# Performance work log

Hardware: AMD Instinct MI355X
Metric: run time of the kernel (lower is better)

Reference implementation:

```python
import jax, jax.numpy as jnp
import numpy as np

N_NODES = 500_000
N_EDGES = 1_000_000
EMB = 64           # config.Model.embedding_size
F = 128            # config.Model.latency_feature_size
L = 8              # config.Latency.latency_feature_length
OP_CNT = 5000
SV_CNT = 2000
ST_CNT = 16
IN_DIM = 3 * EMB + L  # 200


def setup_inputs() -> dict:
    key = jax.random.key(0)
    ks = jax.random.split(key, 24)
    s = 0.02
    inp = {
        'operation_id': jax.random.randint(ks[0], (N_NODES,), 0, OP_CNT, dtype=jnp.int32),
        'service_id':   jax.random.randint(ks[1], (N_NODES,), 0, SV_CNT, dtype=jnp.int32),
        'status_id':    jax.random.randint(ks[2], (N_NODES,), 0, ST_CNT, dtype=jnp.int32),
        'latency_feat': jax.random.normal(ks[3], (N_NODES, L), dtype=jnp.float32),
        'edge_src':     jax.random.randint(ks[4], (N_EDGES,), 0, N_NODES, dtype=jnp.int32),
        'edge_dst':     jax.random.randint(ks[5], (N_EDGES,), 0, N_NODES, dtype=jnp.int32),
        'eps':          jax.random.normal(ks[6], (N_NODES, F), dtype=jnp.float32),
        # parameters (LevelEmbedding + TreeLSTMLatencyEncoder + TreeLSTMLatencyDecoder)
        'op_embed':      jax.random.normal(ks[7],  (OP_CNT, EMB), dtype=jnp.float32) * s,
        'service_embed': jax.random.normal(ks[8],  (SV_CNT, EMB), dtype=jnp.float32) * s,
        'status_embed':  jax.random.normal(ks[9],  (ST_CNT, EMB), dtype=jnp.float32) * s,
        'enc_W1': jax.random.normal(ks[10], (IN_DIM, F), dtype=jnp.float32) * s,
        'enc_b1': jnp.zeros((F,), dtype=jnp.float32),
        'enc_W2': jax.random.normal(ks[11], (F, 2 * F), dtype=jnp.float32) * s,
        'enc_b2': jnp.zeros((2 * F,), dtype=jnp.float32),
        'dec_Wself': jax.random.normal(ks[12], (F, F), dtype=jnp.float32) * s,
        'dec_Wagg':  jax.random.normal(ks[13], (F, F), dtype=jnp.float32) * s,
        'mu_W': jax.random.normal(ks[14], (F, L), dtype=jnp.float32) * s,
        'mu_b': jnp.zeros((L,), dtype=jnp.float32),
        'lv_W': jax.random.normal(ks[15], (F, L), dtype=jnp.float32) * s,
        'lv_b': jnp.zeros((L,), dtype=jnp.float32),
        'opwise_embed': jax.random.normal(ks[16], (OP_CNT + 1, 2 * L * L), dtype=jnp.float32) * s,
    }
    return inp


def reference(operation_id, service_id, status_id, latency_feat, edge_src, edge_dst, eps,
              op_embed, service_embed, status_embed,
              enc_W1, enc_b1, enc_W2, enc_b2,
              dec_Wself, dec_Wagg, mu_W, mu_b, lv_W, lv_b, opwise_embed):
    N = latency_feat.shape[0]
    # ---- LevelEmbedding: gathers + concat ----
    feats = jnp.concatenate([
        op_embed[operation_id],
        service_embed[service_id],
        status_embed[status_id],
        latency_feat,
    ], axis=-1)  # [N, 3*EMB + L]
    # ---- TreeLSTMLatencyEncoder ----
    h = jax.nn.relu(feats @ enc_W1 + enc_b1)
    y = h @ enc_W2 + enc_b2                       # [N, 2F]
    z_mu, z_lv = jnp.split(y, 2, axis=-1)
    z_lv = jnp.tanh(z_lv)
    z = z_mu + jnp.exp(0.5 * z_lv) * eps          # reparameterize, [N, F]
    # ---- TreeLSTM decoder (one child-sum message-passing step over edges) ----
    agg = jax.ops.segment_sum(z[edge_src], edge_dst, num_segments=N)  # scatter-reduce
    yd = jax.nn.relu(z @ dec_Wself + agg @ dec_Wagg)                  # [N, F]
    mu = yd @ mu_W + mu_b   # [N, L]
    lv = yd @ lv_W + lv_b   # [N, L]
    # op-wise output transform: per-node [1,L] @ [L,L]
    w = opwise_embed[operation_id].reshape(N, L, 2 * L)
    w_mu, w_lv = w[..., :L], w[..., L:]
    mu = jnp.einsum('nl,nlk->nk', mu, w_mu)
    lv = jnp.einsum('nl,nlk->nk', lv, w_lv)
    # ---- latency_loss: gaussian NLL + opid scatter aggregation ----
    label = latency_feat
    loss = (mu - label) ** 2 / (2.0 * jnp.exp(lv) + 1e-7) + 0.5 * lv  # [N, L]
    loss_node = jnp.mean(loss, axis=1)                                 # [N]
    op_loss = jax.ops.segment_sum(loss_node, operation_id, num_segments=OP_CNT)
    op_cnt = jax.ops.segment_sum(jnp.ones((N,), jnp.int32), operation_id, num_segments=OP_CNT)
    lat_loss = jnp.mean(loss_node)
    kl = -0.5 * jnp.mean(z_lv + 1.0 - jnp.exp(z_lv) - z_mu ** 2)
    total = lat_loss + kl
    return (total, op_loss, op_cnt)
```

## Files before the change

### kernel.cpp

```cpp
#include <hip/hip_runtime.h>
#include <math.h>

#define NN 500000
#define NE 1000000
#define OPC 5000
#define NBLK_SCAN 489
#define NBLK ((NN + 127) / 128)

typedef short short8 __attribute__((ext_vector_type(8)));
typedef float f32x4 __attribute__((ext_vector_type(4)));

static __device__ __forceinline__ short f2bf(float f) {
    unsigned u = __builtin_bit_cast(unsigned, f);
    u += 0x7fffu + ((u >> 16) & 1u);
    return (short)(u >> 16);
}
static __device__ __forceinline__ float bf2f(short s) {
    unsigned u = ((unsigned)(unsigned short)s) << 16;
    return __builtin_bit_cast(float, u);
}
static __device__ __forceinline__ short8 cvt8(float4 a, float4 b) {
    short8 r;
    r[0] = f2bf(a.x); r[1] = f2bf(a.y); r[2] = f2bf(a.z); r[3] = f2bf(a.w);
    r[4] = f2bf(b.x); r[5] = f2bf(b.y); r[6] = f2bf(b.z); r[7] = f2bf(b.w);
    return r;
}
static __device__ __forceinline__ short8 ldcvt(const float* p) {
    const float4* p4 = (const float4*)p;
    return cvt8(p4[0], p4[1]);
}

__global__ void prep_kernel(const float* __restrict__ W1, const float* __restrict__ W2,
                            const float* __restrict__ Wself, const float* __restrict__ Wagg,
                            const float* __restrict__ muW, const float* __restrict__ lvW,
                            short* __restrict__ W1s, short* __restrict__ W2s,
                            short* __restrict__ Wds0, short* __restrict__ Wds1,
                            short* __restrict__ HWp)
{
    int idx = blockIdx.x * 256 + threadIdx.x;
    {
        int col = idx >> 8, r = idx & 255;
        int k = ((r >> 3) ^ (col & 7)) * 8 + (r & 7);
        W1s[idx] = (k < 200) ? f2bf(W1[k * 128 + col]) : (short)0;
    }
    {
        int col = idx >> 7, r = idx & 127;
        int k = ((r >> 3) ^ (col & 7)) * 8 + (r & 7);
        W2s[idx] = f2bf(W2[k * 256 + col]);
    }
    if (idx < 128 * 128) {
        int col = idx >> 7, r = idx & 127;
        int k = ((r >> 3) ^ (col & 7)) * 8 + (r & 7);
        Wds0[idx] = f2bf(Wself[k * 128 + col]);
        Wds1[idx] = f2bf(Wagg[k * 128 + col]);
    }
    if (idx < 16 * 128) {
        int n = idx >> 7, k = idx & 127;
        HWp[idx] = (n < 8) ? f2bf(muW[k * 8 + n]) : f2bf(lvW[k * 8 + (n - 8)]);
    }
}

__global__ __launch_bounds__(256, 2) void enc1_mfma(
    const int* __restrict__ op_id, const int* __restrict__ sv_id, const int* __restrict__ st_id,
    const float* __restrict__ lat,
    const float* __restrict__ opE, const float* __restrict__ svE, const float* __restrict__ stE,
    const short* __restrict__ W1s, const float* __restrict__ b1,
    short* __restrict__ h_bf)
{
    __shared__ __align__(16) short Bb[128 * 256];
    const int tid = threadIdx.x;
    const int lane = tid & 63, w = tid >> 6;
    const int m = lane & 15, q = lane >> 4;
    const int bbase = blockIdx.x * 128;
    const int wbase = bbase + w * 32;
    const bool wv = (wbase < NN);

    {
        const short8* g = (const short8*)W1s;
        short8* l = (short8*)Bb;
        #pragma unroll
        for (int i = 0; i < 16; i++) l[tid + 256 * i] = g[tid + 256 * i];
    }
    __syncthreads();

    f32x4 acc[2][8];
    #pragma unroll
    for (int a2 = 0; a2 < 2; a2++)
        #pragma unroll
        for (int nf = 0; nf < 8; nf++) acc[a2][nf] = (f32x4)0.0f;

    if (wv) {
        const int n0 = wbase + m, n1 = wbase + 16 + m;
        const size_t op0 = (size_t)op_id[n0] * 64, op1 = (size_t)op_id[n1] * 64;
        const size_t sv0 = (size_t)sv_id[n0] * 64, sv1 = (size_t)sv_id[n1] * 64;
        const size_t st0 = (size_t)st_id[n0] * 64, st1 = (size_t)st_id[n1] * 64;

        #pragma unroll
        for (int s = 0; s < 7; s++) {
            short8 a0, a1;
            if (s < 2) {
                a0 = ldcvt(opE + op0 + s * 32 + q * 8);
                a1 = ldcvt(opE + op1 + s * 32 + q * 8);
            } else if (s < 4) {
                a0 = ldcvt(svE + sv0 + (s - 2) * 32 + q * 8);
                a1 = ldcvt(svE + sv1 + (s - 2) * 32 + q * 8);
            } else if (s < 6) {
                a0 = ldcvt(stE + st0 + (s - 4) * 32 + q * 8);
                a1 = ldcvt(stE + st1 + (s - 4) * 32 + q * 8);
            } else {
                if (q == 0) {
                    a0 = ldcvt(lat + (size_t)n0 * 8);
                    a1 = ldcvt(lat + (size_t)n1 * 8);
                } else {
                    #pragma unroll
                    for (int i = 0; i < 8; i++) { a0[i] = 0; a1[i] = 0; }
                }
            }
            const int slot = ((4 * s + q) ^ (m & 7)) * 8;
            #pragma unroll
            for (int nf = 0; nf < 8; nf++) {
                const short8 b = *(const short8*)&Bb[(nf * 16 + m) * 256 + slot];
                acc[0][nf] = __builtin_amdgcn_mfma_f32_16x16x32_bf16(a0, b, acc[0][nf], 0, 0, 0);
                acc[1][nf] = __builtin_amdgcn_mfma_f32_16x16x32_bf16(a1, b, acc[1][nf], 0, 0, 0);
            }
        }
    }
    __syncthreads();

    if (wv) {
        #pragma unroll
        for (int nf = 0; nf < 8; nf++) {
            int col = nf * 16 + m;
            float bb = b1[col];
            #pragma unroll
            for (int a2 = 0; a2 < 2; a2++)
                #pragma unroll
                for (int r = 0; r < 4; r++) {
                    int g = w * 32 + a2 * 16 + q * 4 + r;
                    Bb[g * 136 + col] = f2bf(fmaxf(acc[a2][nf][r] + bb, 0.0f));
                }
        }
    }
    __syncthreads();

    {
        int g = tid >> 1, cb = (tid & 1) * 64;
        int node = bbase + g;
        if (node < NN) {
            short8* dst = (short8*)(h_bf + (size_t)node * 128 + cb);
            const short8* src = (const short8*)&Bb[g * 136 + cb];
            #pragma unroll
            for (int i = 0; i < 8; i++) dst[i] = src[i];
        }
    }
}

__global__ __launch_bounds__(256, 2) void enc2_mfma(
    const short* __restrict__ h_bf, const short* __restrict__ W2s, const float* __restrict__ b2,
    const float* __restrict__ eps, short* __restrict__ z_bf, float* __restrict__ kl_sum)
{
    __shared__ __align__(16) short Bb[256 * 128];
    int* ldsI = (int*)Bb;
    const int tid = threadIdx.x;
    const int lane = tid & 63, w = tid >> 6;
    const int m = lane & 15, q = lane >> 4;
    const int bbase = blockIdx.x * 128;
    const int wbase = bbase + w * 32;
    const bool wv = (wbase < NN);

    {
        const short8* g8 = (const short8*)W2s;
        short8* l = (short8*)Bb;
        #pragma unroll
        for (int i = 0; i < 16; i++) l[tid + 256 * i] = g8[tid + 256 * i];
    }
    __syncthreads();

    f32x4 acc[2][16];
    #pragma unroll
    for (int a2 = 0; a2 < 2; a2++)
        #pragma unroll
        for (int nf = 0; nf < 16; nf++) acc[a2][nf] = (f32x4)0.0f;

    if (wv) {
        short8 a[2][4];
        #pragma unroll
        for (int s = 0; s < 4; s++) {
            a[0][s] = *(const short8*)(h_bf + (size_t)(wbase + m) * 128 + s * 32 + q * 8);
            a[1][s] = *(const short8*)(h_bf + (size_t)(wbase + 16 + m) * 128 + s * 32 + q * 8);
        }
        #pragma unroll
        for (int s = 0; s < 4; s++) {
            const int slot = ((4 * s + q) ^ (m & 7)) * 8;
            #pragma unroll
            for (int nf = 0; nf < 16; nf++) {
                const short8 b = *(const short8*)&Bb[(nf * 16 + m) * 128 + slot];
                acc[0][nf] = __builtin_amdgcn_mfma_f32_16x16x32_bf16(a[0][s], b, acc[0][nf], 0, 0, 0);
                acc[1][nf] = __builtin_amdgcn_mfma_f32_16x16x32_bf16(a[1][s], b, acc[1][nf], 0, 0, 0);
            }
        }
    }
    __syncthreads();

    float kll = 0.0f;
    #pragma unroll
    for (int a2 = 0; a2 < 2; a2++) {
        if (wv) {
            #pragma unroll
            for (int nf = 0; nf < 8; nf++) {
                int col = nf * 16 + m;
                float bm = b2[col], bl = b2[col + 128];
                #pragma unroll
                for (int r = 0; r < 4; r++) {
                    float mu = acc[a2][nf][r] + bm;
                    float lr = acc[a2][nf + 8][r] + bl;
                    float e2 = __expf(2.0f * lr);
                    float t  = 1.0f - 2.0f * __builtin_amdgcn_rcpf(e2 + 1.0f);
                    float s  = __expf(0.5f * t);
                    kll += t + 1.0f - s * s - mu * mu;
                    int pk = (int)(unsigned short)f2bf(mu)
                           | ((int)(unsigned short)f2bf(s) << 16);
                    ldsI[(w * 16 + q * 4 + r) * 132 + col] = pk;
                }
            }
        }
        __syncthreads();
        {
            int g = tid >> 2, cb = (tid & 3) * 32;
            int node = bbase + (g >> 4) * 32 + a2 * 16 + (g & 15);
            if (node < NN) {
                const float4* ep = (const float4*)(eps + (size_t)node * 128 + cb);
                const int4*   lp = (const int4*)&ldsI[g * 132 + cb];
                #pragma unroll
                for (int c = 0; c < 4; c++) {
                    int4 va = lp[c * 2], vb = lp[c * 2 + 1];
                    float4 ea = ep[c * 2], eb = ep[c * 2 + 1];
                    short8 o;
                    o[0] = f2bf(fmaf(bf2f((short)(va.x >> 16)), ea.x, bf2f((short)va.x)));
                    o[1] = f2bf(fmaf(bf2f((short)(va.y >> 16)), ea.y, bf2f((short)va.y)));
                    o[2] = f2bf(fmaf(bf2f((short)(va.z >> 16)), ea.z, bf2f((short)va.z)));
                    o[3] = f2bf(fmaf(bf2f((short)(va.w >> 16)), ea.w, bf2f((short)va.w)));
                    o[4] = f2bf(fmaf(bf2f((short)(vb.x >> 16)), eb.x, bf2f((short)vb.x)));
                    o[5] = f2bf(fmaf(bf2f((short)(vb.y >> 16)), eb.y, bf2f((short)vb.y)));
                    o[6] = f2bf(fmaf(bf2f((short)(vb.z >> 16)), eb.z, bf2f((short)vb.z)));
                    o[7] = f2bf(fmaf(bf2f((short)(vb.w >> 16)), eb.w, bf2f((short)vb.w)));
                    *(short8*)(z_bf + (size_t)node * 128 + cb + c * 8) = o;
                }
            }
        }
        __syncthreads();
    }
    #pragma unroll
    for (int off = 32; off > 0; off >>= 1) kll += __shfl_down(kll, off);
    if (lane == 0) atomicAdd(kl_sum, kll);
}

__global__ void hist_kernel(const int* __restrict__ edst, int* __restrict__ cnt)
{
    int e = blockIdx.x * 256 + threadIdx.x;
    if (e < NE) atomicAdd(&cnt[edst[e]], 1);
}

__global__ void scan1_kernel(const int* __restrict__ cnt, int* __restrict__ bsum)
{
    __shared__ int ls[256];
    int b = blockIdx.x, tid = threadIdx.x;
    int idx0 = b * 1024 + tid * 4;
    int s = 0;
    #pragma unroll
    for (int i = 0; i < 4; i++) { int idx = idx0 + i; if (idx < NN) s += cnt[idx]; }
    ls[tid] = s; __syncthreads();
    for (int off = 128; off > 0; off >>= 1) {
        if (tid < off) ls[tid] += ls[tid + off];
        __syncthreads();
    }
    if (tid == 0) bsum[b] = ls[0];
}

__global__ void scan2_kernel(int* __restrict__ bsum, int* __restrict__ rowstart)
{
    __shared__ int ls[512];
    int tid = threadIdx.x;
    int v = (tid < NBLK_SCAN) ? bsum[tid] : 0;
    ls[tid] = v; __syncthreads();
    for (int off = 1; off < 512; off <<= 1) {
        int t = 0;
        if (tid >= off) t = ls[tid - off];
        __syncthreads();
        ls[tid] += t;
        __syncthreads();
    }
    if (tid < NBLK_SCAN) bsum[tid] = (tid == 0) ? 0 : ls[tid - 1];
    if (tid == 0) rowstart[NN] = NE;
}

__global__ void scan3_kernel(const int* __restrict__ cnt, const int* __restrict__ bsum,
                             int* __restrict__ rowstart, int* __restrict__ cursor)
{
    __shared__ int ls[256];
    int b = blockIdx.x, tid = threadIdx.x;
    int idx0 = b * 1024 + tid * 4;
    int v[4]; int s = 0;
    #pragma unroll
    for (int i = 0; i < 4; i++) { int idx = idx0 + i; v[i] = (idx < NN) ? cnt[idx] : 0; s += v[i]; }
    ls[tid] = s; __syncthreads();
    for (int off = 1; off < 256; off <<= 1) {
        int t = 0;
        if (tid >= off) t = ls[tid - off];
        __syncthreads();
        ls[tid] += t;
        __syncthreads();
    }
    int ex = ls[tid] - s + bsum[b];
    #pragma unroll
    for (int i = 0; i < 4; i++) {
        int idx = idx0 + i;
        if (idx < NN) { rowstart[idx] = ex; cursor[idx] = ex; }
        ex += v[i];
    }
}

__global__ void fill_kernel(const int* __restrict__ esrc, const int* __restrict__ edst,
                            int* __restrict__ cursor, int* __restrict__ csr)
{
    int e = blockIdx.x * 256 + threadIdx.x;
    if (e < NE) {
        int pos = atomicAdd(&cursor[edst[e]], 1);
        csr[pos] = esrc[e];
    }
}

__global__ __launch_bounds__(256, 2) void dec_mfma(
    const short* __restrict__ z_bf, const int* __restrict__ rowstart, const int* __restrict__ csr,
    const short* __restrict__ Wds0, const short* __restrict__ Wds1, const short* __restrict__ HWp,
    const float* __restrict__ mub, const float* __restrict__ lvb,
    const float* __restrict__ opwise, const int* __restrict__ op_id,
    const float* __restrict__ lat,
    float* __restrict__ op_loss, float* __restrict__ op_cnt,
    float* __restrict__ loss_sum)
{
    __shared__ __align__(16) short regionA[128 * 128];
    __shared__ __align__(16) char  regionB[32768];
    short* Bb  = (short*)regionB;
    short* hw  = (short*)regionB;
    float* mlv = (float*)(regionB + 4608);

    const int tid = threadIdx.x;
    const int lane = tid & 63, w = tid >> 6;
    const int m = lane & 15, q = lane >> 4;
    const int bbase = blockIdx.x * 128;
    const int wbase = bbase + w * 32;
    const bool wv = (wbase < NN);

    {
        const short8* g = (const short8*)Wds0;
        short8* l = (short8*)Bb;
        #pragma unroll
        for (int i = 0; i < 8; i++) l[tid + 256 * i] = g[tid + 256 * i];
    }
    {
        int nodeL = tid & 127, hh = tid >> 7;
        int n = bbase + nodeL;
        float a[64];
        #pragma unroll
        for (int i = 0; i < 64; i++) a[i] = 0.0f;
        if (n < NN) {
            int r0 = rowstart[n], r1 = rowstart[n + 1];
            for (int e = r0; e < r1; e++) {
                const short8* zp = (const short8*)(z_bf + (size_t)csr[e] * 128 + hh * 64);
                #pragma unroll
                for (int j = 0; j < 8; j++) {
                    short8 v = zp[j];
                    #pragma unroll
                    for (int i = 0; i < 8; i++) a[j * 8 + i] += bf2f(v[i]);
                }
            }
        }
        #pragma unroll
        for (int j = 0; j < 8; j++) {
            int slot = ((hh * 8 + j) ^ (nodeL & 7)) * 8;
            short8 o;
            #pragma unroll
            for (int i = 0; i < 8; i++) o[i] = f2bf(a[j * 8 + i]);
            *(short8*)&regionA[nodeL * 128 + slot] = o;
        }
    }
    __syncthreads();

    f32x4 acc[2][8];
    #pragma unroll
    for (int a2 = 0; a2 < 2; a2++)
        #pragma unroll
        for (int nf = 0; nf < 8; nf++) acc[a2][nf] = (f32x4)0.0f;

    if (wv) {
        short8 az[2][4];
        #pragma unroll
        for (int s = 0; s < 4; s++) {
            az[0][s] = *(const short8*)(z_bf + (size_t)(wbase + m) * 128 + s * 32 + q * 8);
            az[1][s] = *(const short8*)(z_bf + (size_t)(wbase + 16 + m) * 128 + s * 32 + q * 8);
        }
        #pragma unroll
        for (int s = 0; s < 4; s++) {
            const int slot = ((4 * s + q) ^ (m & 7)) * 8;
            #pragma unroll
            for (int nf = 0; nf < 8; nf++) {
                const short8 b = *(const short8*)&Bb[(nf * 16 + m) * 128 + slot];
                acc[0][nf] = __builtin_amdgcn_mfma_f32_16x16x32_bf16(az[0][s], b, acc[0][nf], 0, 0, 0);
                acc[1][nf] = __builtin_amdgcn_mfma_f32_16x16x32_bf16(az[1][s], b, acc[1][nf], 0, 0, 0);
            }
        }
    }
    __syncthreads();

    {
        const short8* g = (const short8*)Wds1;
        short8* l = (short8*)Bb;
        #pragma unroll
        for (int i = 0; i < 8; i++) l[tid + 256 * i] = g[tid + 256 * i];
    }
    __syncthreads();

    if (wv) {
        #pragma unroll
        for (int s = 0; s < 4; s++) {
            const int slot = ((4 * s + q) ^ (m & 7)) * 8;
            const short8 a0 = *(const short8*)&regionA[(w * 32 + m) * 128 + slot];
            const short8 a1 = *(const short8*)&regionA[(w * 32 + 16 + m) * 128 + slot];
            #pragma unroll
            for (int nf = 0; nf < 8; nf++) {
                const short8 b = *(const short8*)&Bb[(nf * 16 + m) * 128 + slot];
                acc[0][nf] = __builtin_amdgcn_mfma_f32_16x16x32_bf16(a0, b, acc[0][nf], 0, 0, 0);
                acc[1][nf] = __builtin_amdgcn_mfma_f32_16x16x32_bf16(a1, b, acc[1][nf], 0, 0, 0);
            }
        }
    }
    __syncthreads();

    if (wv) {
        #pragma unroll
        for (int a2 = 0; a2 < 2; a2++)
            #pragma unroll
            for (int nf = 0; nf < 8; nf++) {
                int c = nf * 2 + (m >> 3);
                #pragma unroll
                for (int r = 0; r < 4; r++) {
                    int node = w * 32 + a2 * 16 + q * 4 + r;
                    regionA[node * 128 + ((c ^ (node & 7)) * 8) + (m & 7)] =
                        f2bf(fmaxf(acc[a2][nf][r], 0.0f));
                }
            }
    }
    {
        int nn = tid >> 4, c = tid & 15;
        *(short8*)&hw[nn * 136 + c * 8] = *(const short8*)(HWp + nn * 128 + c * 8);
    }
    __syncthreads();

    if (wv) {
        f32x4 h0 = (f32x4)0.0f, h1 = (f32x4)0.0f;
        #pragma unroll
        for (int s2 = 0; s2 < 4; s2++) {
            const int slot = ((4 * s2 + q) ^ (m & 7)) * 8;
            short8 a0 = *(const short8*)&regionA[(w * 32 + m) * 128 + slot];
            short8 a1 = *(const short8*)&regionA[(w * 32 + 16 + m) * 128 + slot];
            short8 b  = *(const short8*)&hw[m * 136 + s2 * 32 + q * 8];
            h0 = __builtin_amdgcn_mfma_f32_16x16x32_bf16(a0, b, h0, 0, 0, 0);
            h1 = __builtin_amdgcn_mfma_f32_16x16x32_bf16(a1, b, h1, 0, 0, 0);
        }
        float hb = (m < 8) ? mub[m] : lvb[m - 8];
        #pragma unroll
        for (int r = 0; r < 4; r++) {
            mlv[(w * 32 + q * 4 + r) * 16 + m]      = h0[r] + hb;
            mlv[(w * 32 + 16 + q * 4 + r) * 16 + m] = h1[r] + hb;
        }
    }
    __syncthreads();

    float lsum = 0.0f;
    if (tid < 128 && bbase + tid < NN) {
        const int t = tid;
        const int n = bbase + t;
        const int op = op_id[n];
        const float4* w4 = (const float4*)(opwise + (size_t)op * 128);
        float mout[8], lout[8];
        #pragma unroll
        for (int k = 0; k < 8; k++) { mout[k] = 0.0f; lout[k] = 0.0f; }
        #pragma unroll
        for (int l = 0; l < 8; l++) {
            float mv = mlv[t * 16 + l];
            float vv = mlv[t * 16 + 8 + l];
            float4 a = w4[l * 4 + 0];
            float4 b = w4[l * 4 + 1];
            float4 c = w4[l * 4 + 2];
            float4 d = w4[l * 4 + 3];
            mout[0] = fmaf(mv, a.x, mout[0]); mout[1] = fmaf(mv, a.y, mout[1]);
            mout[2] = fmaf(mv, a.z, mout[2]); mout[3] = fmaf(mv, a.w, mout[3]);
            mout[4] = fmaf(mv, b.x, mout[4]); mout[5] = fmaf(mv, b.y, mout[5]);
            mout[6] = fmaf(mv, b.z, mout[6]); mout[7] = fmaf(mv, b.w, mout[7]);
            lout[0] = fmaf(vv, c.x, lout[0]); lout[1] = fmaf(vv, c.y, lout[1]);
            lout[2] = fmaf(vv, c.z, lout[2]); lout[3] = fmaf(vv, c.w, lout[3]);
            lout[4] = fmaf(vv, d.x, lout[4]); lout[5] = fmaf(vv, d.y, lout[5]);
            lout[6] = fmaf(vv, d.z, lout[6]); lout[7] = fmaf(vv, d.w, lout[7]);
        }
        const float4* lp = (const float4*)(lat + (size_t)n * 8);
        float4 lb0 = lp[0], lb1 = lp[1];
        float labels[8] = {lb0.x, lb0.y, lb0.z, lb0.w, lb1.x, lb1.y, lb1.z, lb1.w};
        float lnode = 0.0f;
        #pragma unroll
        for (int k = 0; k < 8; k++) {
            float diff = mout[k] - labels[k];
            lnode += diff * diff / (2.0f * expf(lout[k]) + 1e-7f) + 0.5f * lout[k];
        }
        lnode *= 0.125f;
        atomicAdd(&op_loss[op], lnode);
        atomicAdd(&op_cnt[op], 1.0f);
        lsum = lnode;
    }
    #pragma unroll
    for (int off = 32; off > 0; off >>= 1) lsum += __shfl_down(lsum, off);
    if (lane == 0) atomicAdd(loss_sum, lsum);
}

__global__ void final_kernel(const float* __restrict__ accum, float* __restrict__ out)
{
    out[0] = accum[1] / (float)NN - 0.5f * (accum[0] / (float)((size_t)NN * 128));
}

extern "C" void kernel_launch(void* const* d_in, const int* in_sizes, int n_in,
                              void* d_out, int out_size, void* d_ws, size_t ws_size,
                              hipStream_t stream) {
    const int*   op_id  = (const int*)  d_in[0];
    const int*   sv_id  = (const int*)  d_in[1];
    const int*   st_id  = (const int*)  d_in[2];
    const float* lat    = (const float*)d_in[3];
    const int*   esrc   = (const int*)  d_in[4];
    const int*   edst   = (const int*)  d_in[5];
    const float* eps    = (const float*)d_in[6];
    const float* opE    = (const float*)d_in[7];
    const float* svE    = (const float*)d_in[8];
    const float* stE    = (const float*)d_in[9];
    const float* W1     = (const float*)d_in[10];
    const float* b1     = (const float*)d_in[11];
    const float* W2     = (const float*)d_in[12];
    const float* b2     = (const float*)d_in[13];
    const float* Wself  = (const float*)d_in[14];
    const float* Wagg   = (const float*)d_in[15];
    const float* muW    = (const float*)d_in[16];
    const float* mub    = (const float*)d_in[17];
    const float* lvW    = (const float*)d_in[18];
    const float* lvb    = (const float*)d_in[19];
    const float* opwise = (const float*)d_in[20];

    char* wsb = (char*)d_ws;
    short* W1s      = (short*)(wsb + 0);
    short* W2s      = (short*)(wsb + 65536);
    short* Wds0     = (short*)(wsb + 131072);
    short* Wds1     = (short*)(wsb + 163840);
    short* HWp      = (short*)(wsb + 196608);
    float* accum    = (float*)(wsb + 204800);
    int*   cnt      = (int*)  (wsb + (4  << 20));
    int*   rowstart = (int*)  (wsb + (6  << 20));
    int*   cursor   = (int*)  (wsb + (9  << 20));
    int*   csr      = (int*)  (wsb + (12 << 20));
    int*   bsum     = (int*)  (wsb + (16 << 20));
    short* h_bf     = (short*)(wsb + (32  << 20));
    short* z_bf     = (short*)(wsb + (160ull << 20));
    float* out      = (float*)d_out;

    hipMemsetAsync(d_out, 0, (size_t)out_size * sizeof(float), stream);
    hipMemsetAsync(accum, 0, 2 * sizeof(float), stream);
    hipMemsetAsync(cnt, 0, (size_t)NN * sizeof(int), stream);

    prep_kernel<<<128, 256, 0, stream>>>(W1, W2, Wself, Wagg, muW, lvW,
                                         W1s, W2s, Wds0, Wds1, HWp);

    hist_kernel<<<(NE + 255) / 256, 256, 0, stream>>>(edst, cnt);
    scan1_kernel<<<NBLK_SCAN, 256, 0, stream>>>(cnt, bsum);
    scan2_kernel<<<1, 512, 0, stream>>>(bsum, rowstart);
    scan3_kernel<<<NBLK_SCAN, 256, 0, stream>>>(cnt, bsum, rowstart, cursor);
    fill_kernel<<<(NE + 255) / 256, 256, 0, stream>>>(esrc, edst, cursor, csr);

    enc1_mfma<<<NBLK, 256, 0, stream>>>(op_id, sv_id, st_id, lat, opE, svE, stE, W1s, b1, h_bf);
    enc2_mfma<<<NBLK, 256, 0, stream>>>(h_bf, W2s, b2, eps, z_bf, accum + 0);
    dec_mfma<<<NBLK, 256, 0, stream>>>(z_bf, rowstart, csr, Wds0, Wds1, HWp, mub, lvb,
                                       opwise, op_id, lat,
                                       out + 1, out + 1 + OPC, accum + 1);
    final_kernel<<<1, 1, 0, stream>>>(accum, out);
}
```

Before: 1.047 ms.

## Pre-swizzle weights into MFMA fragment order and read B directly from global/L2

The weight-prep kernel now lays out each bf16 weight matrix in per-lane MFMA B-fragment order. The encoder and decoder kernels load B operands straight from global memory (L2-resident) instead of staging whole weight matrices into LDS, which drops the staging loops and several block barriers. With LDS use reduced, launch bounds go from 2 to 4 blocks per CU to raise occupancy. The cost is that every wave refetches the weights from cache, and the global loads add latency to the MFMA loops.

```diff
diff --git a/kernel.cpp b/kernel.cpp
--- a/kernel.cpp
+++ b/kernel.cpp
@@ -33,55 +33,49 @@
 __global__ void prep_kernel(const float* __restrict__ W1, const float* __restrict__ W2,
                             const float* __restrict__ Wself, const float* __restrict__ Wagg,
                             const float* __restrict__ muW, const float* __restrict__ lvW,
-                            short* __restrict__ W1s, short* __restrict__ W2s,
-                            short* __restrict__ Wds0, short* __restrict__ Wds1,
-                            short* __restrict__ HWp)
+                            short* __restrict__ W1f, short* __restrict__ W2f,
+                            short* __restrict__ Wf0, short* __restrict__ Wf1,
+                            short* __restrict__ HWf)
 {
     int idx = blockIdx.x * 256 + threadIdx.x;
+    int j = idx & 7, lane = (idx >> 3) & 63;
+    int m = lane & 15, q = lane >> 4;
     {
-        int col = idx >> 8, r = idx & 255;
-        int k = ((r >> 3) ^ (col & 7)) * 8 + (r & 7);
-        W1s[idx] = (k < 200) ? f2bf(W1[k * 128 + col]) : (short)0;
+        int s = idx >> 12, nf = (idx >> 9) & 7;
+        int k = s * 32 + q * 8 + j, col = nf * 16 + m;
+        W1f[idx] = (k < 200) ? f2bf(W1[k * 128 + col]) : (short)0;
     }
     {
-        int col = idx >> 7, r = idx & 127;
-        int k = ((r >> 3) ^ (col & 7)) * 8 + (r & 7);
-        W2s[idx] = f2bf(W2[k * 256 + col]);
-    }
-    if (idx < 128 * 128) {
-        int col = idx >> 7, r = idx & 127;
-        int k = ((r >> 3) ^ (col & 7)) * 8 + (r & 7);
-        Wds0[idx] = f2bf(Wself[k * 128 + col]);
-        Wds1[idx] = f2bf(Wagg[k * 128 + col]);
-    }
-    if (idx < 16 * 128) {
-        int n = idx >> 7, k = idx & 127;
-        HWp[idx] = (n < 8) ? f2bf(muW[k * 8 + n]) : f2bf(lvW[k * 8 + (n - 8)]);
-    }
-}
-
-__global__ __launch_bounds__(256, 2) void enc1_mfma(
+        int s = idx >> 13, nf = (idx >> 9) & 15;
+        int k = s * 32 + q * 8 + j, col = nf * 16 + m;
+        W2f[idx] = f2bf(W2[k * 256 + col]);
+    }
+    if (idx < 16384) {
+        int s = idx >> 12, nf = (idx >> 9) & 7;
+        int k = s * 32 + q * 8 + j, col = nf * 16 + m;
+        Wf0[idx] = f2bf(Wself[k * 128 + col]);
+        Wf1[idx] = f2bf(Wagg[k * 128 + col]);
+    }
+    if (idx < 2048) {
+        int k = (idx >> 9) * 32 + q * 8 + j;
+        HWf[idx] = (m < 8) ? f2bf(muW[k * 8 + m]) : f2bf(lvW[k * 8 + (m - 8)]);
+    }
+}
+
+__global__ __launch_bounds__(256, 4) void enc1_mfma(
     const int* __restrict__ op_id, const int* __restrict__ sv_id, const int* __restrict__ st_id,
     const float* __restrict__ lat,
     const float* __restrict__ opE, const float* __restrict__ svE, const float* __restrict__ stE,
-    const short* __restrict__ W1s, const float* __restrict__ b1,
+    const short* __restrict__ W1f, const float* __restrict__ b1,
     short* __restrict__ h_bf)
 {
-    __shared__ __align__(16) short Bb[128 * 256];
+    __shared__ __align__(16) short Hs[128 * 136];
     const int tid = threadIdx.x;
     const int lane = tid & 63, w = tid >> 6;
     const int m = lane & 15, q = lane >> 4;
     const int bbase = blockIdx.x * 128;
     const int wbase = bbase + w * 32;
     const bool wv = (wbase < NN);
-
-    {
-        const short8* g = (const short8*)W1s;
-        short8* l = (short8*)Bb;
-        #pragma unroll
-        for (int i = 0; i < 16; i++) l[tid + 256 * i] = g[tid + 256 * i];
-    }
-    __syncthreads();
 
     f32x4 acc[2][8];
     #pragma unroll
@@ -116,16 +110,14 @@
                     for (int i = 0; i < 8; i++) { a0[i] = 0; a1[i] = 0; }
                 }
             }
-            const int slot = ((4 * s + q) ^ (m & 7)) * 8;
             #pragma unroll
             for (int nf = 0; nf < 8; nf++) {
-                const short8 b = *(const short8*)&Bb[(nf * 16 + m) * 256 + slot];
+                const short8 b = *(const short8*)(W1f + (s * 8 + nf) * 512 + lane * 8);
                 acc[0][nf] = __builtin_amdgcn_mfma_f32_16x16x32_bf16(a0, b, acc[0][nf], 0, 0, 0);
                 acc[1][nf] = __builtin_amdgcn_mfma_f32_16x16x32_bf16(a1, b, acc[1][nf], 0, 0, 0);
             }
         }
     }
-    __syncthreads();
 
     if (wv) {
         #pragma unroll
@@ -137,7 +129,7 @@
                 #pragma unroll
                 for (int r = 0; r < 4; r++) {
                     int g = w * 32 + a2 * 16 + q * 4 + r;
-                    Bb[g * 136 + col] = f2bf(fmaxf(acc[a2][nf][r] + bb, 0.0f));
+                    Hs[g * 136 + col] = f2bf(fmaxf(acc[a2][nf][r] + bb, 0.0f));
                 }
         }
     }
@@ -148,19 +140,18 @@
         int node = bbase + g;
         if (node < NN) {
             short8* dst = (short8*)(h_bf + (size_t)node * 128 + cb);
-            const short8* src = (const short8*)&Bb[g * 136 + cb];
+            const short8* src = (const short8*)&Hs[g * 136 + cb];
             #pragma unroll
             for (int i = 0; i < 8; i++) dst[i] = src[i];
         }
     }
 }
 
-__global__ __launch_bounds__(256, 2) void enc2_mfma(
-    const short* __restrict__ h_bf, const short* __restrict__ W2s, const float* __restrict__ b2,
+__global__ __launch_bounds__(256, 4) void enc2_mfma(
+    const short* __restrict__ h_bf, const short* __restrict__ W2f, const float* __restrict__ b2,
     const float* __restrict__ eps, short* __restrict__ z_bf, float* __restrict__ kl_sum)
 {
-    __shared__ __align__(16) short Bb[256 * 128];
-    int* ldsI = (int*)Bb;
+    __shared__ __align__(16) int ldsI[64 * 132];
     const int tid = threadIdx.x;
     const int lane = tid & 63, w = tid >> 6;
     const int m = lane & 15, q = lane >> 4;
@@ -168,14 +159,6 @@
     const int wbase = bbase + w * 32;
     const bool wv = (wbase < NN);
 
-    {
-        const short8* g8 = (const short8*)W2s;
-        short8* l = (short8*)Bb;
-        #pragma unroll
-        for (int i = 0; i < 16; i++) l[tid + 256 * i] = g8[tid + 256 * i];
-    }
-    __syncthreads();
-
     f32x4 acc[2][16];
     #pragma unroll
     for (int a2 = 0; a2 < 2; a2++)
@@ -191,16 +174,14 @@
         }
         #pragma unroll
         for (int s = 0; s < 4; s++) {
-            const int slot = ((4 * s + q) ^ (m & 7)) * 8;
             #pragma unroll
             for (int nf = 0; nf < 16; nf++) {
-                const short8 b = *(const short8*)&Bb[(nf * 16 + m) * 128 + slot];
+                const short8 b = *(const short8*)(W2f + (s * 16 + nf) * 512 + lane * 8);
                 acc[0][nf] = __builtin_amdgcn_mfma_f32_16x16x32_bf16(a[0][s], b, acc[0][nf], 0, 0, 0);
                 acc[1][nf] = __builtin_amdgcn_mfma_f32_16x16x32_bf16(a[1][s], b, acc[1][nf], 0, 0, 0);
             }
         }
     }
-    __syncthreads();
 
     float kll = 0.0f;
     #pragma unroll
@@ -330,9 +311,9 @@
     }
 }
 
-__global__ __launch_bounds__(256, 2) void dec_mfma(
+__global__ __launch_bounds__(256, 4) void dec_mfma(
     const short* __restrict__ z_bf, const int* __restrict__ rowstart, const int* __restrict__ csr,
-    const short* __restrict__ Wds0, const short* __restrict__ Wds1, const short* __restrict__ HWp,
+    const short* __restrict__ Wf0, const short* __restrict__ Wf1, const short* __restrict__ HWf,
     const float* __restrict__ mub, const float* __restrict__ lvb,
     const float* __restrict__ opwise, const int* __restrict__ op_id,
     const float* __restrict__ lat,
@@ -340,10 +321,7 @@
     float* __restrict__ loss_sum)
 {
     __shared__ __align__(16) short regionA[128 * 128];
-    __shared__ __align__(16) char  regionB[32768];
-    short* Bb  = (short*)regionB;
-    short* hw  = (short*)regionB;
-    float* mlv = (float*)(regionB + 4608);
+    float* mlv = (float*)regionA;
 
     const int tid = threadIdx.x;
     const int lane = tid & 63, w = tid >> 6;
@@ -352,12 +330,6 @@
     const int wbase = bbase + w * 32;
     const bool wv = (wbase < NN);
 
-    {
-        const short8* g = (const short8*)Wds0;
-        short8* l = (short8*)Bb;
-        #pragma unroll
-        for (int i = 0; i < 8; i++) l[tid + 256 * i] = g[tid + 256 * i];
-    }
     {
         int nodeL = tid & 127, hh = tid >> 7;
         int n = bbase + nodeL;
@@ -393,6 +365,8 @@
         #pragma unroll
         for (int nf = 0; nf < 8; nf++) acc[a2][nf] = (f32x4)0.0f;
 
+    f32x4 h0 = (f32x4)0.0f, h1 = (f32x4)0.0f;
+
     if (wv) {
         short8 az[2][4];
         #pragma unroll
@@ -402,26 +376,14 @@
         }
         #pragma unroll
         for (int s = 0; s < 4; s++) {
-            const int slot = ((4 * s + q) ^ (m & 7)) * 8;
             #pragma unroll
             for (int nf = 0; nf < 8; nf++) {
-                const short8 b = *(const short8*)&Bb[(nf * 16 + m) * 128 + slot];
+                const short8 b = *(const short8*)(Wf0 + (s * 8 + nf) * 512 + lane * 8);
                 acc[0][nf] = __builtin_amdgcn_mfma_f32_16x16x32_bf16(az[0][s], b, acc[0][nf], 0, 0, 0);
                 acc[1][nf] = __builtin_amdgcn_mfma_f32_16x16x32_bf16(az[1][s], b, acc[1][nf], 0, 0, 0);
             }
         }
-    }
-    __syncthreads();
-
-    {
-        const short8* g = (const short8*)Wds1;
-        short8* l = (short8*)Bb;
-        #pragma unroll
-        for (int i = 0; i < 8; i++) l[tid + 256 * i] = g[tid + 256 * i];
-    }
-    __syncthreads();
-
-    if (wv) {
+
         #pragma unroll
         for (int s = 0; s < 4; s++) {
             const int slot = ((4 * s + q) ^ (m & 7)) * 8;
@@ -429,15 +391,12 @@
             const short8 a1 = *(const short8*)&regionA[(w * 32 + 16 + m) * 128 + slot];
             #pragma unroll
             for (int nf = 0; nf < 8; nf++) {
-                const short8 b = *(const short8*)&Bb[(nf * 16 + m) * 128 + slot];
+                const short8 b = *(const short8*)(Wf1 + (s * 8 + nf) * 512 + lane * 8);
                 acc[0][nf] = __builtin_amdgcn_mfma_f32_16x16x32_bf16(a0, b, acc[0][nf], 0, 0, 0);
                 acc[1][nf] = __builtin_amdgcn_mfma_f32_16x16x32_bf16(a1, b, acc[1][nf], 0, 0, 0);
             }
         }
-    }
-    __syncthreads();
-
-    if (wv) {
+
         #pragma unroll
         for (int a2 = 0; a2 < 2; a2++)
             #pragma unroll
@@ -450,29 +409,25 @@
                         f2bf(fmaxf(acc[a2][nf][r], 0.0f));
                 }
             }
-    }
-    {
-        int nn = tid >> 4, c = tid & 15;
-        *(short8*)&hw[nn * 136 + c * 8] = *(const short8*)(HWp + nn * 128 + c * 8);
-    }
-    __syncthreads();
-
-    if (wv) {
-        f32x4 h0 = (f32x4)0.0f, h1 = (f32x4)0.0f;
+
         #pragma unroll
         for (int s2 = 0; s2 < 4; s2++) {
             const int slot = ((4 * s2 + q) ^ (m & 7)) * 8;
             short8 a0 = *(const short8*)&regionA[(w * 32 + m) * 128 + slot];
             short8 a1 = *(const short8*)&regionA[(w * 32 + 16 + m) * 128 + slot];
-            short8 b  = *(const short8*)&hw[m * 136 + s2 * 32 + q * 8];
+            short8 b  = *(const short8*)(HWf + s2 * 512 + lane * 8);
             h0 = __builtin_amdgcn_mfma_f32_16x16x32_bf16(a0, b, h0, 0, 0, 0);
             h1 = __builtin_amdgcn_mfma_f32_16x16x32_bf16(a1, b, h1, 0, 0, 0);
         }
+    }
+    __syncthreads();
+
+    if (wv) {
         float hb = (m < 8) ? mub[m] : lvb[m - 8];
         #pragma unroll
         for (int r = 0; r < 4; r++) {
-            mlv[(w * 32 + q * 4 + r) * 16 + m]      = h0[r] + hb;
-            mlv[(w * 32 + 16 + q * 4 + r) * 16 + m] = h1[r] + hb;
+            mlv[(w * 32 + q * 4 + r) * 17 + m]      = h0[r] + hb;
+            mlv[(w * 32 + 16 + q * 4 + r) * 17 + m] = h1[r] + hb;
         }
     }
     __syncthreads();
@@ -488,8 +443,8 @@
         for (int k = 0; k < 8; k++) { mout[k] = 0.0f; lout[k] = 0.0f; }
         #pragma unroll
         for (int l = 0; l < 8; l++) {
-            float mv = mlv[t * 16 + l];
-            float vv = mlv[t * 16 + 8 + l];
+            float mv = mlv[t * 17 + l];
+            float vv = mlv[t * 17 + 8 + l];
             float4 a = w4[l * 4 + 0];
             float4 b = w4[l * 4 + 1];
             float4 c = w4[l * 4 + 2];
@@ -553,11 +508,11 @@
     const float* opwise = (const float*)d_in[20];
 
     char* wsb = (char*)d_ws;
-    short* W1s      = (short*)(wsb + 0);
-    short* W2s      = (short*)(wsb + 65536);
-    short* Wds0     = (short*)(wsb + 131072);
-    short* Wds1     = (short*)(wsb + 163840);
-    short* HWp      = (short*)(wsb + 196608);
+    short* W1f      = (short*)(wsb + 0);
+    short* W2f      = (short*)(wsb + 65536);
+    short* Wf0      = (short*)(wsb + 131072);
+    short* Wf1      = (short*)(wsb + 163840);
+    short* HWf      = (short*)(wsb + 196608);
     float* accum    = (float*)(wsb + 204800);
     int*   cnt      = (int*)  (wsb + (4  << 20));
     int*   rowstart = (int*)  (wsb + (6  << 20));
@@ -573,7 +528,7 @@
     hipMemsetAsync(cnt, 0, (size_t)NN * sizeof(int), stream);
 
     prep_kernel<<<128, 256, 0, stream>>>(W1, W2, Wself, Wagg, muW, lvW,
-                                         W1s, W2s, Wds0, Wds1, HWp);
+                                         W1f, W2f, Wf0, Wf1, HWf);
 
     hist_kernel<<<(NE + 255) / 256, 256, 0, stream>>>(edst, cnt);
     scan1_kernel<<<NBLK_SCAN, 256, 0, stream>>>(cnt, bsum);
@@ -581,9 +536,9 @@
     scan3_kernel<<<NBLK_SCAN, 256, 0, stream>>>(cnt, bsum, rowstart, cursor);
     fill_kernel<<<(NE + 255) / 256, 256, 0, stream>>>(esrc, edst, cursor, csr);
 
-    enc1_mfma<<<NBLK, 256, 0, stream>>>(op_id, sv_id, st_id, lat, opE, svE, stE, W1s, b1, h_bf);
-    enc2_mfma<<<NBLK, 256, 0, stream>>>(h_bf, W2s, b2, eps, z_bf, accum + 0);
-    dec_mfma<<<NBLK, 256, 0, stream>>>(z_bf, rowstart, csr, Wds0, Wds1, HWp, mub, lvb,
+    enc1_mfma<<<NBLK, 256, 0, stream>>>(op_id, sv_id, st_id, lat, opE, svE, stE, W1f, b1, h_bf);
+    enc2_mfma<<<NBLK, 256, 0, stream>>>(h_bf, W2f, b2, eps, z_bf, accum + 0);
+    dec_mfma<<<NBLK, 256, 0, stream>>>(z_bf, rowstart, csr, Wf0, Wf1, HWf, mub, lvb,
                                        opwise, op_id, lat,
                                        out + 1, out + 1 + OPC, accum + 1);
     final_kernel<<<1, 1, 0, stream>>>(accum, out);
```

Measured after the change: 1.210 ms. 15.6% more time.
